# Kernel optimization log

Measured on AMD Instinct MI355X. Metric: run time of the kernel, lower is better.

## Reference

```python
import jax, jax.numpy as jnp
import numpy as np

B, T, L = 64, 512, 48
START, PAD, END = 46, 45, 47


def setup_inputs() -> dict:
    key = jax.random.key(0)
    k1, k2, k3 = jax.random.split(key, 3)
    scores = jax.random.normal(k1, (B, T, L), dtype=jnp.float32)
    gold_target = jax.random.randint(k2, (B, T), 0, L, dtype=jnp.int64)
    trans = jax.random.normal(k3, (L, L), dtype=jnp.float32)
    # replicate the in-place constraint initialization from __init__ (order matters)
    trans = trans.at[:, START].set(-10000.0)
    trans = trans.at[END, :].set(-10000.0)
    trans = trans.at[PAD, :].set(-10000.0)
    trans = trans.at[PAD, END].set(0.0)
    trans = trans.at[PAD, PAD].set(0.0)
    trans = trans.at[START, :].set(0.0)
    mask = jnp.ones((B, T), dtype=jnp.int32)
    return {"scores": scores, "gold_target": gold_target, "mask": mask, "transitions": trans}


def reference(scores, gold_target, mask, transitions):
    Bn, Tn, Ln = scores.shape
    # crf_scores[t, b, from, to] = emission(b, t, from) + transitions[from, to]  (time-major)
    crf = scores.transpose(1, 0, 2)[:, :, :, None] + transitions[None, None]      # (T, B, L, L)
    start = jnp.broadcast_to(transitions[None, None], (1, Bn, Ln, Ln))
    crf = jnp.concatenate([start, crf], axis=0)                                   # (T+1, B, L, L)

    # gold energy: faithful to original torch.gather on flattened (L*L) with raw tag index
    gold = jnp.concatenate(
        [jnp.full((1, Bn), START, dtype=gold_target.dtype), gold_target.T], axis=0)  # (T+1, B)
    flat = crf.reshape(Tn + 1, Bn, Ln * Ln)
    tg = jnp.take_along_axis(flat, gold[:, :, None], axis=2)[:, :, 0]             # (T+1, B)
    maskp = jnp.concatenate([jnp.ones((1, Bn), mask.dtype), mask.T], axis=0)      # (T+1, B)
    tg_energy = jnp.sum(tg * maskp.astype(tg.dtype))

    # forward algorithm (stable log-sum-exp recurrence) via lax.scan
    init = crf[0, :, START, :]                                                    # (B, L)
    def step(fs, xs):
        trans_t, m_t = xs                                                         # (B,L,L), (B,)
        nxt = jax.nn.logsumexp(fs[:, :, None] + trans_t, axis=1)                  # (B, L)
        fs = jnp.where(m_t[:, None].astype(bool), nxt, fs)
        return fs, None
    fs, _ = jax.lax.scan(step, init, (crf[1:], maskp[1:]))
    forscore = fs[:, END].sum()

    return (forscore - tg_energy) / Bn
```

## Files before the change

### kernel.cpp

```cpp
#include <hip/hip_runtime.h>

#define Bn 64
#define Tn 512
#define Ln 48
#define START_L 46
#define PAD_L 45
#define END_L 47
#define QP 72
#define LSEG 16
#define NSEG 8
#define NCHUNK (Tn / (LSEG * NSEG))

typedef __bf16 bf16x8 __attribute__((ext_vector_type(8)));
typedef float f32x4 __attribute__((ext_vector_type(4)));
#define MFMA __builtin_amdgcn_mfma_f32_16x16x32_bf16

__device__ __forceinline__ unsigned short f2bf(float x) {
    unsigned u = __float_as_uint(x);
    u += 0x7fffu + ((u >> 16) & 1u);
    return (unsigned short)(u >> 16);
}
__device__ __forceinline__ unsigned pkT(float a, float b) {
    return __builtin_amdgcn_perm(__float_as_uint(b), __float_as_uint(a), 0x07060302u);
}
__device__ __forceinline__ float bcast0(float x) {
    return __int_as_float(__builtin_amdgcn_readfirstlane(__float_as_int(x)));
}
__device__ __forceinline__ float4 exp4(float4 v) {
    float4 r; r.x = __expf(v.x); r.y = __expf(v.y); r.z = __expf(v.z); r.w = __expf(v.w);
    return r;
}
__device__ __forceinline__ float sexp(float x) {
    return __int_as_float((int)fmaf(x, 12102203.0f, 1064866805.0f));
}
__device__ __forceinline__ float4 fexp4(float4 v) {
    float4 r; r.x = sexp(v.x); r.y = sexp(v.y); r.z = sexp(v.z); r.w = sexp(v.w);
    return r;
}


__device__ __forceinline__ void readTB(const unsigned short* buf, int c, int q, bf16x8 F[3][2]) {
    #pragma unroll
    for (int x = 0; x < 3; ++x) {
        F[x][0] = *(const bf16x8*)&buf[(x * 16 + c) * QP + q * 8];
        F[x][1] = *(const bf16x8*)&buf[(x * 16 + c) * QP + 32 + q * 8];
    }
}

__device__ __forceinline__ void storeTB(unsigned short* buf, int c, int q,
                                        const f32x4 (&acc)[3][3],
                                        float4 w0, float4 w1, float4 w2) {
    #pragma unroll
    for (int nt = 0; nt < 3; ++nt) {
        unsigned u0 = pkT(acc[0][nt][0] * w0.x, acc[0][nt][1] * w0.y);
        unsigned u1 = pkT(acc[0][nt][2] * w0.z, acc[0][nt][3] * w0.w);
        unsigned u2 = pkT(acc[1][nt][0] * w1.x, acc[1][nt][1] * w1.y);
        unsigned u3 = pkT(acc[1][nt][2] * w1.z, acc[1][nt][3] * w1.w);
        unsigned u4 = pkT(acc[2][nt][0] * w2.x, acc[2][nt][1] * w2.y);
        unsigned u5 = pkT(acc[2][nt][2] * w2.z, acc[2][nt][3] * w2.w);
        unsigned short* wp = &buf[(nt * 16 + c) * QP + q * 16];
        uint4 s4; s4.x = u0; s4.y = u1; s4.z = u2; s4.w = u3;
        *(uint4*)wp = s4;
        uint2 s2; s2.x = u4; s2.y = u5;
        *(uint2*)(wp + 8) = s2;
    }
}

__device__ __forceinline__ float treeProd(const unsigned short* bufA, const unsigned short* bufB,
                                          unsigned short* dst, int c, int q) {
    bf16x8 FA[3][2], FB[3][2];
    readTB(bufA, c, q, FA);
    readTB(bufB, c, q, FB);
    f32x4 acc[3][3];
    const f32x4 z = {0.f, 0.f, 0.f, 0.f};
    #pragma unroll
    for (int mt = 0; mt < 3; ++mt)
        #pragma unroll
        for (int nt = 0; nt < 3; ++nt) {
            acc[mt][nt] = MFMA(FA[mt][0], FB[nt][0], z, 0, 0, 0);
            acc[mt][nt] = MFMA(FA[mt][1], FB[nt][1], acc[mt][nt], 0, 0, 0);
        }
    float r = bcast0(acc[0][0][0]);
    float rr = __builtin_amdgcn_rcpf(r);
    float4 w; w.x = rr; w.y = rr; w.z = rr; w.w = rr;
    storeTB(dst, c, q, acc, w, w, w);
    return __logf(r);
}

__global__ __launch_bounds__(512, 2) void scan_k(
        const float* __restrict__ scores,
        const float* __restrict__ trans,
        unsigned short* __restrict__ ws2M,
        float* __restrict__ ws2S,
        float* __restrict__ out) {
    const int b   = blockIdx.x & (Bn - 1);
    const int cid = blockIdx.x >> 6;
    const int tid = threadIdx.x;
    const int w   = tid >> 6;
    const int lane = tid & 63;
    const int c = lane & 15;
    const int q = lane >> 4;

    __shared__ __align__(16) unsigned short TBs[NSEG][48 * QP];
    __shared__ float scl[16];

    for (int i = tid; i < NSEG * 48 * QP / 4; i += 512)
        ((unsigned long long*)TBs)[i] = 0ull;
    __syncthreads();

    const int s    = cid * NSEG + w;
    const int t0   = s * LSEG;
    const int tend = t0 + LSEG - 1;
    const int dirOdd = w & 1;
    const float* sb = scores + (size_t)b * Tn * Ln;

    bf16x8 A[3][2];
    #pragma unroll
    for (int mt = 0; mt < 3; ++mt)
        #pragma unroll
        for (int kt = 0; kt < 2; ++kt) {
            union { unsigned u[4]; bf16x8 v; } fu;
            #pragma unroll
            for (int j2 = 0; j2 < 4; ++j2) {
                int kk0 = kt * 32 + q * 8 + 2 * j2;
                int rem = kk0 & 15;
                if (rem < 12) {
                    int row0 = (rem >> 2) * 16 + (kk0 >> 4) * 4 + (kk0 & 3);
                    float tv0 = dirOdd ? trans[(mt * 16 + c) * Ln + row0]
                                       : trans[row0 * Ln + mt * 16 + c];
                    float tv1 = dirOdd ? trans[(mt * 16 + c) * Ln + row0 + 1]
                                       : trans[(row0 + 1) * Ln + mt * 16 + c];
                    fu.u[j2] = pkT(__expf(tv0), __expf(tv1));
                } else fu.u[j2] = 0u;
            }
            A[mt][kt] = fu.v;
        }

    unsigned short* myTB = TBs[w];

    if (lane < Ln) {
        int m16 = lane >> 4, q4 = (lane >> 2) & 3, r = lane & 3;
        int kk = q4 * 16 + m16 * 4 + r;
        myTB[lane * QP + kk] = dirOdd ? (unsigned short)0x3F80
                                      : f2bf(__expf(sb[(size_t)t0 * Ln + lane]));
    }

    float4 wA, wB, wC, rA, rB, rC;
    {
        int t1 = dirOdd ? tend : (t0 + 1);
        const float* rp = sb + (size_t)t1 * Ln;
        wA = fexp4(*(const float4*)(rp + q * 4));
        wB = fexp4(*(const float4*)(rp + 16 + q * 4));
        wC = fexp4(*(const float4*)(rp + 32 + q * 4));
        int t2 = dirOdd ? (tend - 1) : (t0 + 2);
        const float* rp2 = sb + (size_t)t2 * Ln;
        rA = *(const float4*)(rp2 + q * 4);
        rB = *(const float4*)(rp2 + 16 + q * 4);
        rC = *(const float4*)(rp2 + 32 + q * 4);
    }

    f32x4 acc[3][3];
    float Cs = 0.f;
    for (int tau = 0; tau < LSEG; ++tau) {
        bf16x8 Bf[3][2];
        readTB(myTB, c, q, Bf);

        int tp = dirOdd ? (tend - (tau + 2)) : (t0 + 3 + tau);
        if (tp < t0) tp = t0;
        if (tp > tend) tp = tend;
        const float* rp3 = sb + (size_t)tp * Ln;
        float4 nA = *(const float4*)(rp3 + q * 4);
        float4 nB = *(const float4*)(rp3 + 16 + q * 4);
        float4 nC = *(const float4*)(rp3 + 32 + q * 4);

        const f32x4 z = {0.f, 0.f, 0.f, 0.f};
        #pragma unroll
        for (int mt = 0; mt < 3; ++mt)
            #pragma unroll
            for (int nt = 0; nt < 3; ++nt) {
                acc[mt][nt] = MFMA(A[mt][0], Bf[nt][0], z, 0, 0, 0);
                acc[mt][nt] = MFMA(A[mt][1], Bf[nt][1], acc[mt][nt], 0, 0, 0);
            }

        float4 w0 = wA, w1 = wB, w2 = wC;
        if (!dirOdd && tau == LSEG - 1) {
            w0.x = w0.y = w0.z = w0.w = 1.f; w1 = w0; w2 = w0;
        }
        if ((tau & 3) == 0) {
            float r = bcast0(acc[0][0][0]);
            float rr = __builtin_amdgcn_rcpf(r);
            Cs += __logf(r);
            w0.x *= rr; w0.y *= rr; w0.z *= rr; w0.w *= rr;
            w1.x *= rr; w1.y *= rr; w1.z *= rr; w1.w *= rr;
            w2.x *= rr; w2.y *= rr; w2.z *= rr; w2.w *= rr;
        }
        storeTB(myTB, c, q, acc, w0, w1, w2);

        wA = fexp4(rA); wB = fexp4(rB); wC = fexp4(rC);
        rA = nA; rB = nB; rC = nC;
    }
    if (lane == 0) scl[w] = Cs;
    __syncthreads();

    if (w < 4) {
        const unsigned short* bufA = TBs[(w & 1) ? (2 * w) : (2 * w + 1)];
        const unsigned short* bufB = TBs[(w & 1) ? (2 * w + 1) : (2 * w)];
        float lg = treeProd(bufA, bufB, TBs[2 * w], c, q);
        if (lane == 0) scl[8 + w] = lg;
    }
    __syncthreads();
    if (w < 2) {
        const unsigned short* bufA = TBs[w ? 4 : 2];
        const unsigned short* bufB = TBs[w ? 6 : 0];
        float lg = treeProd(bufA, bufB, TBs[w ? 4 : 0], c, q);
        if (lane == 0) scl[12 + w] = lg;
    }
    __syncthreads();
    if (w == 0) {
        bf16x8 FA[3][2], FB[3][2];
        readTB(TBs[4], c, q, FA);
        readTB(TBs[0], c, q, FB);
        f32x4 pac[3][3];
        const f32x4 z = {0.f, 0.f, 0.f, 0.f};
        #pragma unroll
        for (int mt = 0; mt < 3; ++mt)
            #pragma unroll
            for (int nt = 0; nt < 3; ++nt) {
                pac[mt][nt] = MFMA(FA[mt][0], FB[nt][0], z, 0, 0, 0);
                pac[mt][nt] = MFMA(FA[mt][1], FB[nt][1], pac[mt][nt], 0, 0, 0);
            }
        float r = bcast0(pac[0][0][0]);
        float rr = __builtin_amdgcn_rcpf(r);
        float Ct = __logf(r);
        #pragma unroll
        for (int i2 = 0; i2 < 14; ++i2) Ct += scl[i2];
        unsigned short* mp = ws2M + (size_t)blockIdx.x * (Ln * Ln);
        #pragma unroll
        for (int mt = 0; mt < 3; ++mt)
            #pragma unroll
            for (int nt = 0; nt < 3; ++nt)
                #pragma unroll
                for (int r2 = 0; r2 < 4; ++r2)
                    mp[(mt * 16 + q * 4 + r2) * Ln + nt * 16 + c] = f2bf(pac[mt][nt][r2] * rr);
        if (lane == 0) ws2S[blockIdx.x] = Ct;
    }
    if (blockIdx.x == 0 && tid == 0) out[0] = 0.f;
}

__global__ __launch_bounds__(256) void fin_k(
        const float* __restrict__ scores,
        const int* __restrict__ gold,
        const int* __restrict__ mask,
        const float* __restrict__ trans,
        const unsigned short* __restrict__ ws2M,
        const float* __restrict__ ws2S,
        float* __restrict__ out) {
    const int b = blockIdx.x;
    const int tid = threadIdx.x;
    const int wv = tid >> 6;
    const int lane = tid & 63;

    __shared__ float vB[64];
    __shared__ float gred[4];

    float tgv = 0.0f;
    #pragma unroll
    for (int k = 0; k < 2; ++k) {
        int idx = b * Tn + tid + k * 256;
        if (mask[idx]) tgv += scores[(size_t)idx * Ln] + trans[gold[idx]];
    }
    #pragma unroll
    for (int off = 32; off > 0; off >>= 1) tgv += __shfl_down(tgv, off);
    if (lane == 0) gred[wv] = tgv;
    __syncthreads();
    if (tid == 0) {
        float s = gred[0] + gred[1] + gred[2] + gred[3];
        float vv = -s * (1.0f / Bn);
        if (b == 0) vv -= trans[START_L];
        atomicAdd(out, vv);
    }

    if (wv == 0) {
        const int j = (lane < Ln) ? lane : (Ln - 1);
        float v = (lane < Ln) ? __expf(trans[START_L * Ln + lane]) : 0.0f;
        float Ctot = 0.0f;

        uint4 rows[NCHUNK][6];
        #pragma unroll
        for (int s2 = 0; s2 < NCHUNK; ++s2) {
            const unsigned short* p = ws2M + (size_t)(s2 * Bn + b) * (Ln * Ln) + (size_t)j * Ln;
            #pragma unroll
            for (int k = 0; k < 6; ++k) rows[s2][k] = *(const uint4*)(p + k * 8);
        }

        #pragma unroll
        for (int s2 = 0; s2 < NCHUNK; ++s2) {
            float Cs = ws2S[s2 * Bn + b];
            if (lane < Ln) vB[lane] = v;

            float a0 = 0.f, a1 = 0.f, a2 = 0.f, a3 = 0.f;
            #pragma unroll
            for (int k2 = 0; k2 < 12; ++k2) {
                float4 vb = *(const float4*)&vB[k2 * 4];
                uint4 ch = rows[s2][k2 >> 1];
                unsigned d0 = (k2 & 1) ? ch.z : ch.x;
                unsigned d1 = (k2 & 1) ? ch.w : ch.y;
                float f0 = __uint_as_float(d0 << 16);
                float f1 = __uint_as_float(d0 & 0xffff0000u);
                float f2 = __uint_as_float(d1 << 16);
                float f3 = __uint_as_float(d1 & 0xffff0000u);
                a0 = fmaf(f0, vb.x, a0);
                a1 = fmaf(f1, vb.y, a1);
                a2 = fmaf(f2, vb.z, a2);
                a3 = fmaf(f3, vb.w, a3);
            }
            float accv = (a0 + a1) + (a2 + a3);

            float r = bcast0(accv);
            v = accv * __builtin_amdgcn_rcpf(r);
            Ctot += __logf(r) + Cs;
        }

        if (lane == END_L) {
            atomicAdd(out, (__logf(v) + Ctot) * (1.0f / Bn));
        }
    }
}

extern "C" void kernel_launch(void* const* d_in, const int* in_sizes, int n_in,
                              void* d_out, int out_size, void* d_ws, size_t ws_size,
                              hipStream_t stream) {
    const float* scores = (const float*)d_in[0];
    const int*   gold   = (const int*)d_in[1];
    const int*   mask   = (const int*)d_in[2];
    const float* trans  = (const float*)d_in[3];
    float* out = (float*)d_out;

    unsigned short* ws2M = (unsigned short*)d_ws;
    float* ws2S = (float*)((char*)d_ws + (size_t)Bn * NCHUNK * Ln * Ln * 2);

    scan_k<<<Bn * NCHUNK, 512, 0, stream>>>(scores, trans, ws2M, ws2S, out);
    fin_k<<<Bn, 256, 0, stream>>>(scores, gold, mask, trans, ws2M, ws2S, out);
}
```

Before: 83.33 us.

## Keep CRF transfer matrices in registers using 16x16x16 MFMA layout

Switches from the 16x16x32 bf16 MFMA with padded LDS tiles to the 16x16x16 variant, whose accumulator layout matches its B-operand layout. The running 48x48 segment product can then stay in registers across time steps instead of round-tripping through shared memory each step. This removes the LDS zero-init, the per-step LDS writes and reads, and the padding waste of the K=32 tiling (48 now splits exactly into three K=16 tiles). It trades this for 27 smaller MFMAs per step instead of 18 larger ones, and the tree reduction now uses a compact per-lane LDS layout.

```diff
diff --git a/kernel.cpp b/kernel.cpp
--- a/kernel.cpp
+++ b/kernel.cpp
@@ -6,14 +6,13 @@
 #define START_L 46
 #define PAD_L 45
 #define END_L 47
-#define QP 72
 #define LSEG 16
 #define NSEG 8
 #define NCHUNK (Tn / (LSEG * NSEG))
 
-typedef __bf16 bf16x8 __attribute__((ext_vector_type(8)));
 typedef float f32x4 __attribute__((ext_vector_type(4)));
-#define MFMA __builtin_amdgcn_mfma_f32_16x16x32_bf16
+typedef short s16x4 __attribute__((ext_vector_type(4)));
+#define MFMA16(a, b, c) __builtin_amdgcn_mfma_f32_16x16x16bf16_1k(a, b, c, 0, 0, 0)
 
 __device__ __forceinline__ unsigned short f2bf(float x) {
     unsigned u = __float_as_uint(x);
@@ -26,10 +25,6 @@
 __device__ __forceinline__ float bcast0(float x) {
     return __int_as_float(__builtin_amdgcn_readfirstlane(__float_as_int(x)));
 }
-__device__ __forceinline__ float4 exp4(float4 v) {
-    float4 r; r.x = __expf(v.x); r.y = __expf(v.y); r.z = __expf(v.z); r.w = __expf(v.w);
-    return r;
-}
 __device__ __forceinline__ float sexp(float x) {
     return __int_as_float((int)fmaf(x, 12102203.0f, 1064866805.0f));
 }
@@ -38,52 +33,38 @@
     return r;
 }
 
-
-__device__ __forceinline__ void readTB(const unsigned short* buf, int c, int q, bf16x8 F[3][2]) {
-    #pragma unroll
-    for (int x = 0; x < 3; ++x) {
-        F[x][0] = *(const bf16x8*)&buf[(x * 16 + c) * QP + q * 8];
-        F[x][1] = *(const bf16x8*)&buf[(x * 16 + c) * QP + 32 + q * 8];
-    }
-}
-
-__device__ __forceinline__ void storeTB(unsigned short* buf, int c, int q,
-                                        const f32x4 (&acc)[3][3],
-                                        float4 w0, float4 w1, float4 w2) {
-    #pragma unroll
-    for (int nt = 0; nt < 3; ++nt) {
-        unsigned u0 = pkT(acc[0][nt][0] * w0.x, acc[0][nt][1] * w0.y);
-        unsigned u1 = pkT(acc[0][nt][2] * w0.z, acc[0][nt][3] * w0.w);
-        unsigned u2 = pkT(acc[1][nt][0] * w1.x, acc[1][nt][1] * w1.y);
-        unsigned u3 = pkT(acc[1][nt][2] * w1.z, acc[1][nt][3] * w1.w);
-        unsigned u4 = pkT(acc[2][nt][0] * w2.x, acc[2][nt][1] * w2.y);
-        unsigned u5 = pkT(acc[2][nt][2] * w2.z, acc[2][nt][3] * w2.w);
-        unsigned short* wp = &buf[(nt * 16 + c) * QP + q * 16];
-        uint4 s4; s4.x = u0; s4.y = u1; s4.z = u2; s4.w = u3;
-        *(uint4*)wp = s4;
-        uint2 s2; s2.x = u4; s2.y = u5;
-        *(uint2*)(wp + 8) = s2;
-    }
-}
-
-__device__ __forceinline__ float treeProd(const unsigned short* bufA, const unsigned short* bufB,
-                                          unsigned short* dst, int c, int q) {
-    bf16x8 FA[3][2], FB[3][2];
-    readTB(bufA, c, q, FA);
-    readTB(bufB, c, q, FB);
+union U2 { unsigned u[2]; uint2 p; s16x4 v; };
+
+
+__device__ __forceinline__ float treeProd16(const uint2 (*TA)[64], const uint2 (*TBp)[64],
+                                            uint2 (*TDst)[64], int lane) {
+    s16x4 FA[9], FB[9];
+    #pragma unroll
+    for (int t = 0; t < 9; ++t) {
+        U2 a; a.p = TA[t][lane];  FA[t] = a.v;
+        U2 b; b.p = TBp[t][lane]; FB[t] = b.v;
+    }
+    const f32x4 z = {0.f, 0.f, 0.f, 0.f};
     f32x4 acc[3][3];
-    const f32x4 z = {0.f, 0.f, 0.f, 0.f};
-    #pragma unroll
-    for (int mt = 0; mt < 3; ++mt)
-        #pragma unroll
-        for (int nt = 0; nt < 3; ++nt) {
-            acc[mt][nt] = MFMA(FA[mt][0], FB[nt][0], z, 0, 0, 0);
-            acc[mt][nt] = MFMA(FA[mt][1], FB[nt][1], acc[mt][nt], 0, 0, 0);
+    #pragma unroll
+    for (int i = 0; i < 3; ++i)
+        #pragma unroll
+        for (int j = 0; j < 3; ++j) {
+            f32x4 a = MFMA16(FA[0 * 3 + i], FB[0 * 3 + j], z);
+            a = MFMA16(FA[1 * 3 + i], FB[1 * 3 + j], a);
+            acc[i][j] = MFMA16(FA[2 * 3 + i], FB[2 * 3 + j], a);
         }
     float r = bcast0(acc[0][0][0]);
     float rr = __builtin_amdgcn_rcpf(r);
-    float4 w; w.x = rr; w.y = rr; w.z = rr; w.w = rr;
-    storeTB(dst, c, q, acc, w, w, w);
+    #pragma unroll
+    for (int i = 0; i < 3; ++i)
+        #pragma unroll
+        for (int j = 0; j < 3; ++j) {
+            U2 pu;
+            pu.u[0] = pkT(acc[i][j][0] * rr, acc[i][j][1] * rr);
+            pu.u[1] = pkT(acc[i][j][2] * rr, acc[i][j][3] * rr);
+            TDst[i * 3 + j][lane] = pu.p;
+        }
     return __logf(r);
 }
 
@@ -101,12 +82,8 @@
     const int c = lane & 15;
     const int q = lane >> 4;
 
-    __shared__ __align__(16) unsigned short TBs[NSEG][48 * QP];
+    __shared__ uint2 TD[NSEG][9][64];
     __shared__ float scl[16];
-
-    for (int i = tid; i < NSEG * 48 * QP / 4; i += 512)
-        ((unsigned long long*)TBs)[i] = 0ull;
-    __syncthreads();
 
     const int s    = cid * NSEG + w;
     const int t0   = s * LSEG;
@@ -114,36 +91,37 @@
     const int dirOdd = w & 1;
     const float* sb = scores + (size_t)b * Tn * Ln;
 
-    bf16x8 A[3][2];
-    #pragma unroll
-    for (int mt = 0; mt < 3; ++mt)
-        #pragma unroll
-        for (int kt = 0; kt < 2; ++kt) {
-            union { unsigned u[4]; bf16x8 v; } fu;
-            #pragma unroll
-            for (int j2 = 0; j2 < 4; ++j2) {
-                int kk0 = kt * 32 + q * 8 + 2 * j2;
-                int rem = kk0 & 15;
-                if (rem < 12) {
-                    int row0 = (rem >> 2) * 16 + (kk0 >> 4) * 4 + (kk0 & 3);
-                    float tv0 = dirOdd ? trans[(mt * 16 + c) * Ln + row0]
-                                       : trans[row0 * Ln + mt * 16 + c];
-                    float tv1 = dirOdd ? trans[(mt * 16 + c) * Ln + row0 + 1]
-                                       : trans[(row0 + 1) * Ln + mt * 16 + c];
-                    fu.u[j2] = pkT(__expf(tv0), __expf(tv1));
-                } else fu.u[j2] = 0u;
-            }
-            A[mt][kt] = fu.v;
-        }
-
-    unsigned short* myTB = TBs[w];
-
-    if (lane < Ln) {
-        int m16 = lane >> 4, q4 = (lane >> 2) & 3, r = lane & 3;
-        int kk = q4 * 16 + m16 * 4 + r;
-        myTB[lane * QP + kk] = dirOdd ? (unsigned short)0x3F80
-                                      : f2bf(__expf(sb[(size_t)t0 * Ln + lane]));
-    }
+    s16x4 AT[3][3];
+    #pragma unroll
+    for (int kt = 0; kt < 3; ++kt)
+        #pragma unroll
+        for (int it = 0; it < 3; ++it) {
+            U2 au;
+            #pragma unroll
+            for (int p2 = 0; p2 < 2; ++p2) {
+                int a0 = q * 4 + 2 * p2;
+                float tv0 = dirOdd ? trans[(it * 16 + c) * Ln + kt * 16 + a0]
+                                   : trans[(kt * 16 + a0) * Ln + it * 16 + c];
+                float tv1 = dirOdd ? trans[(it * 16 + c) * Ln + kt * 16 + a0 + 1]
+                                   : trans[(kt * 16 + a0 + 1) * Ln + it * 16 + c];
+                au.u[p2] = pkT(__expf(tv0), __expf(tv1));
+            }
+            AT[kt][it] = au.v;
+        }
+
+    s16x4 YB[3][3];
+    #pragma unroll
+    for (int k = 0; k < 3; ++k)
+        #pragma unroll
+        for (int j = 0; j < 3; ++j) {
+            U2 yu; yu.u[0] = 0u; yu.u[1] = 0u;
+            if (k == j && q == (c >> 2)) {
+                unsigned short hv = dirOdd ? (unsigned short)0x3F80
+                                           : f2bf(__expf(sb[(size_t)t0 * Ln + k * 16 + c]));
+                yu.u[(c >> 1) & 1] = ((unsigned)hv) << ((c & 1) * 16);
+            }
+            YB[k][j] = yu.v;
+        }
 
     float4 wA, wB, wC, rA, rB, rC;
     {
@@ -159,12 +137,9 @@
         rC = *(const float4*)(rp2 + 32 + q * 4);
     }
 
-    f32x4 acc[3][3];
+    const f32x4 z = {0.f, 0.f, 0.f, 0.f};
     float Cs = 0.f;
     for (int tau = 0; tau < LSEG; ++tau) {
-        bf16x8 Bf[3][2];
-        readTB(myTB, c, q, Bf);
-
         int tp = dirOdd ? (tend - (tau + 2)) : (t0 + 3 + tau);
         if (tp < t0) tp = t0;
         if (tp > tend) tp = tend;
@@ -173,13 +148,14 @@
         float4 nB = *(const float4*)(rp3 + 16 + q * 4);
         float4 nC = *(const float4*)(rp3 + 32 + q * 4);
 
-        const f32x4 z = {0.f, 0.f, 0.f, 0.f};
-        #pragma unroll
-        for (int mt = 0; mt < 3; ++mt)
-            #pragma unroll
-            for (int nt = 0; nt < 3; ++nt) {
-                acc[mt][nt] = MFMA(A[mt][0], Bf[nt][0], z, 0, 0, 0);
-                acc[mt][nt] = MFMA(A[mt][1], Bf[nt][1], acc[mt][nt], 0, 0, 0);
+        f32x4 acc[3][3];
+        #pragma unroll
+        for (int i = 0; i < 3; ++i)
+            #pragma unroll
+            for (int j = 0; j < 3; ++j) {
+                f32x4 a = MFMA16(AT[0][i], YB[0][j], z);
+                a = MFMA16(AT[1][i], YB[1][j], a);
+                acc[i][j] = MFMA16(AT[2][i], YB[2][j], a);
             }
 
         float4 w0 = wA, w1 = wB, w2 = wC;
@@ -194,40 +170,59 @@
             w1.x *= rr; w1.y *= rr; w1.z *= rr; w1.w *= rr;
             w2.x *= rr; w2.y *= rr; w2.z *= rr; w2.w *= rr;
         }
-        storeTB(myTB, c, q, acc, w0, w1, w2);
+        #pragma unroll
+        for (int i = 0; i < 3; ++i) {
+            float4 wi = (i == 0) ? w0 : (i == 1) ? w1 : w2;
+            #pragma unroll
+            for (int j = 0; j < 3; ++j) {
+                U2 pu;
+                pu.u[0] = pkT(acc[i][j][0] * wi.x, acc[i][j][1] * wi.y);
+                pu.u[1] = pkT(acc[i][j][2] * wi.z, acc[i][j][3] * wi.w);
+                YB[i][j] = pu.v;
+            }
+        }
 
         wA = fexp4(rA); wB = fexp4(rB); wC = fexp4(rC);
         rA = nA; rB = nB; rC = nC;
     }
     if (lane == 0) scl[w] = Cs;
+
+    #pragma unroll
+    for (int i = 0; i < 3; ++i)
+        #pragma unroll
+        for (int j = 0; j < 3; ++j) {
+            U2 du; du.v = YB[i][j];
+            TD[w][i * 3 + j][lane] = du.p;
+        }
     __syncthreads();
 
     if (w < 4) {
-        const unsigned short* bufA = TBs[(w & 1) ? (2 * w) : (2 * w + 1)];
-        const unsigned short* bufB = TBs[(w & 1) ? (2 * w + 1) : (2 * w)];
-        float lg = treeProd(bufA, bufB, TBs[2 * w], c, q);
+        int ia = (w & 1) ? (2 * w) : (2 * w + 1);
+        int ib = (w & 1) ? (2 * w + 1) : (2 * w);
+        float lg = treeProd16(TD[ia], TD[ib], TD[2 * w], lane);
         if (lane == 0) scl[8 + w] = lg;
     }
     __syncthreads();
     if (w < 2) {
-        const unsigned short* bufA = TBs[w ? 4 : 2];
-        const unsigned short* bufB = TBs[w ? 6 : 0];
-        float lg = treeProd(bufA, bufB, TBs[w ? 4 : 0], c, q);
+        float lg = treeProd16(TD[w ? 4 : 2], TD[w ? 6 : 0], TD[w ? 4 : 0], lane);
         if (lane == 0) scl[12 + w] = lg;
     }
     __syncthreads();
     if (w == 0) {
-        bf16x8 FA[3][2], FB[3][2];
-        readTB(TBs[4], c, q, FA);
-        readTB(TBs[0], c, q, FB);
+        s16x4 FA[9], FB[9];
+        #pragma unroll
+        for (int t = 0; t < 9; ++t) {
+            U2 a; a.p = TD[4][t][lane];  FA[t] = a.v;
+            U2 bb; bb.p = TD[0][t][lane]; FB[t] = bb.v;
+        }
         f32x4 pac[3][3];
-        const f32x4 z = {0.f, 0.f, 0.f, 0.f};
-        #pragma unroll
-        for (int mt = 0; mt < 3; ++mt)
-            #pragma unroll
-            for (int nt = 0; nt < 3; ++nt) {
-                pac[mt][nt] = MFMA(FA[mt][0], FB[nt][0], z, 0, 0, 0);
-                pac[mt][nt] = MFMA(FA[mt][1], FB[nt][1], pac[mt][nt], 0, 0, 0);
+        #pragma unroll
+        for (int i = 0; i < 3; ++i)
+            #pragma unroll
+            for (int j = 0; j < 3; ++j) {
+                f32x4 a = MFMA16(FA[0 * 3 + i], FB[0 * 3 + j], z);
+                a = MFMA16(FA[1 * 3 + i], FB[1 * 3 + j], a);
+                pac[i][j] = MFMA16(FA[2 * 3 + i], FB[2 * 3 + j], a);
             }
         float r = bcast0(pac[0][0][0]);
         float rr = __builtin_amdgcn_rcpf(r);
```

Measured after the change: 82.98 us. No clear change (-0.4%).
